# Optimization experiments

Hardware: AMD Instinct MI355X
Metric: run time of the kernel (lower is better)

## Reference

```python
import jax, jax.numpy as jnp
import numpy as np

INPUT, HIDDEN, C, H, W, PK = 64, 128, 16, 32, 32, 4
B, T = 512, 1024

def hardsigmoid(v):
    return jnp.clip(v / 6.0 + 0.5, 0.0, 1.0)

def setup_inputs() -> dict:
    key = jax.random.key(0)
    ks = jax.random.split(key, 9)
    s_rnn = 1.0 / np.sqrt(HIDDEN)
    s_map = 1.0 / np.sqrt(HIDDEN)
    return {
        "x": jax.random.normal(ks[0], (B, T, INPUT), dtype=jnp.float32),
        "W_ih": jax.random.uniform(ks[1], (HIDDEN, INPUT), minval=-s_rnn, maxval=s_rnn),
        "b_ih": jax.random.uniform(ks[2], (HIDDEN,), minval=-s_rnn, maxval=s_rnn),
        "W_hh": jax.random.uniform(ks[3], (HIDDEN, HIDDEN), minval=-s_rnn, maxval=s_rnn),
        "b_hh": jax.random.uniform(ks[4], (HIDDEN,), minval=-s_rnn, maxval=s_rnn),
        "W_gate": jax.random.uniform(ks[5], (HIDDEN, HIDDEN), minval=-s_rnn, maxval=s_rnn),
        "b_gate": jax.random.uniform(ks[6], (HIDDEN,), minval=-s_rnn, maxval=s_rnn),
        "W_map": jax.random.uniform(ks[7], (C * H * W, HIDDEN), minval=-s_map, maxval=s_map),
        "b_map": jax.random.uniform(ks[8], (C * H * W,), minval=-s_map, maxval=s_map),
    }

def reference(x, W_ih, b_ih, W_hh, b_hh, W_gate, b_gate, W_map, b_map):
    batch, seq_len, _ = x.shape
    h0 = jnp.zeros((batch, HIDDEN), dtype=x.dtype)
    agg0 = jnp.zeros((batch, HIDDEN), dtype=x.dtype)

    def step(carry, xt):
        h, agg = carry
        h = jnp.tanh(xt @ W_ih.T + b_ih + h @ W_hh.T + b_hh)
        gate = hardsigmoid(h @ W_gate.T + b_gate)
        return (h, agg + h * gate), None

    (h, agg), _ = jax.lax.scan(step, (h0, agg0), jnp.swapaxes(x, 0, 1))
    agg = agg / float(seq_len)

    mapped = (agg @ W_map.T + b_map).reshape(batch, C, H, W)
    # AvgPool2d(kernel=PK, stride=PK) via reshape-mean
    pooled = mapped.reshape(batch, C, H // PK, PK, W // PK, PK).mean(axis=(3, 5))
    upsampled = jnp.repeat(jnp.repeat(pooled, PK, axis=2), PK, axis=3)
    return mapped * hardsigmoid(upsampled)
```

## Files before the change

### kernel.cpp

```cpp
#include <hip/hip_runtime.h>
#include <hip/hip_bf16.h>

#define T_SEQ 1024
#define BATCH 512
#define INPUT 64
#define HID   128

typedef __attribute__((ext_vector_type(8))) short bf16x8;
typedef __attribute__((ext_vector_type(4))) short s16x4;
typedef __attribute__((ext_vector_type(4))) float f32x4;

__device__ __forceinline__ short f2bf(float f) {
    union { float f; unsigned u; } v; v.f = f;
    unsigned r = (v.u + 0x7FFFu + ((v.u >> 16) & 1u)) >> 16;
    return (short)r;
}

__device__ __forceinline__ float fast_tanh(float s) {
    float e = __expf(2.0f * s);
    return 1.0f - 2.0f * __builtin_amdgcn_rcpf(e + 1.0f);
}

__device__ __forceinline__ float hsig(float v) {
    return __builtin_amdgcn_fmed3f(v * 0.16666666666666666f + 0.5f, 0.0f, 1.0f);
}

__device__ __forceinline__ void wg_barrier_lds() {
    asm volatile("s_waitcnt lgkmcnt(0)" ::: "memory");
    __builtin_amdgcn_s_barrier();
    asm volatile("" ::: "memory");
}

__global__ __launch_bounds__(256) void cvt_kernel(const float* __restrict__ in,
                                                  short* __restrict__ out, int n4) {
    int i = blockIdx.x * 256 + threadIdx.x;
    if (i >= n4) return;
    f32x4 v = ((const f32x4*)in)[i];
    s16x4 o;
    #pragma unroll
    for (int j = 0; j < 4; ++j) o[j] = f2bf(v[j]);
    ((s16x4*)out)[i] = o;
}

template<bool PRE>
__global__ __launch_bounds__(512, 2) void rnn_kernel(
    const float* __restrict__ xf, const short* __restrict__ xb,
    const float* __restrict__ W_ih, const float* __restrict__ b_ih,
    const float* __restrict__ W_hh, const float* __restrict__ b_hh,
    const float* __restrict__ W_gate, const float* __restrict__ b_gate,
    float* __restrict__ agg_out)
{
    __shared__ short sh0[16][136];
    __shared__ short sh1[16][136];

    const int tid  = threadIdx.x;
    const int wave = tid >> 6, lane = tid & 63;
    const int q = lane >> 4, l15 = lane & 15;
    const int b0 = blockIdx.x * 16;
    const int n0 = wave * 16;
    const int n  = n0 + l15;

    bf16x8 w1[6], wg[4];
    #pragma unroll
    for (int kb = 0; kb < 6; ++kb) {
        const float* p = (kb < 2) ? (W_ih + n * INPUT + kb * 32 + q * 8)
                                  : (W_hh + n * HID + (kb - 2) * 32 + q * 8);
        bf16x8 f;
        #pragma unroll
        for (int j = 0; j < 8; ++j) f[j] = f2bf(p[j]);
        w1[kb] = f;
    }
    #pragma unroll
    for (int kb = 0; kb < 4; ++kb) {
        const float* p = W_gate + n * HID + kb * 32 + q * 8;
        bf16x8 f;
        #pragma unroll
        for (int j = 0; j < 8; ++j) f[j] = f2bf(p[j]);
        wg[kb] = f;
    }
    const float b1 = b_ih[n] + b_hh[n], bgv = b_gate[n];
    f32x4 bias1v, biasgv, zero4;
    #pragma unroll
    for (int r = 0; r < 4; ++r) { bias1v[r] = b1; biasgv[r] = bgv; zero4[r] = 0.0f; }

    f32x4 agg = zero4;
    float hp0 = 0.f, hp1 = 0.f, hp2 = 0.f, hp3 = 0.f;
    bf16x8 hf0, hf1, hf2, hf3;
    #pragma unroll
    for (int j = 0; j < 8; ++j) { hf0[j] = 0; hf1[j] = 0; hf2[j] = 0; hf3[j] = 0; }

    bf16x8 xaE0, xaE1, xaO0, xaO1;
    const short* xq = nullptr;
    const float* xqf = nullptr;
    if (PRE) {
        const short* xp = xb + ((long)(b0 + l15) * T_SEQ) * INPUT + q * 8;
        xaE0 = *(const bf16x8*)(xp);
        xaE1 = *(const bf16x8*)(xp + 32);
        xaO0 = *(const bf16x8*)(xp + INPUT);
        xaO1 = *(const bf16x8*)(xp + INPUT + 32);
        xq = xp + 2 * INPUT;
    } else {
        const float* xp = xf + ((long)(b0 + l15) * T_SEQ) * INPUT + q * 8;
        f32x4 a0 = *(const f32x4*)(xp),          a1 = *(const f32x4*)(xp + 4);
        f32x4 a2 = *(const f32x4*)(xp + 32),     a3 = *(const f32x4*)(xp + 36);
        f32x4 c0 = *(const f32x4*)(xp + 64),     c1 = *(const f32x4*)(xp + 68);
        f32x4 c2 = *(const f32x4*)(xp + 96),     c3 = *(const f32x4*)(xp + 100);
        #pragma unroll
        for (int j = 0; j < 4; ++j) {
            xaE0[j] = f2bf(a0[j]); xaE0[4 + j] = f2bf(a1[j]);
            xaE1[j] = f2bf(a2[j]); xaE1[4 + j] = f2bf(a3[j]);
            xaO0[j] = f2bf(c0[j]); xaO0[4 + j] = f2bf(c1[j]);
            xaO1[j] = f2bf(c2[j]); xaO1[4 + j] = f2bf(c3[j]);
        }
        xqf = xp + 2 * INPUT;
    }

    f32x4 accx;
    accx = __builtin_amdgcn_mfma_f32_16x16x32_bf16(xaE0, w1[0], bias1v, 0, 0, 0);
    accx = __builtin_amdgcn_mfma_f32_16x16x32_bf16(xaE1, w1[1], accx, 0, 0, 0);

    for (int i = 0; i < T_SEQ / 2; ++i) {
        {
            const int t = 2 * i;
            if (PRE) {
                xaE0 = *(const bf16x8*)(xq);
                xaE1 = *(const bf16x8*)(xq + 32);
                if (t < T_SEQ - 3) xq += INPUT;
            } else {
                f32x4 a0 = *(const f32x4*)(xqf),      a1 = *(const f32x4*)(xqf + 4);
                f32x4 a2 = *(const f32x4*)(xqf + 32), a3 = *(const f32x4*)(xqf + 36);
                #pragma unroll
                for (int j = 0; j < 4; ++j) {
                    xaE0[j] = f2bf(a0[j]); xaE0[4 + j] = f2bf(a1[j]);
                    xaE1[j] = f2bf(a2[j]); xaE1[4 + j] = f2bf(a3[j]);
                }
                if (t < T_SEQ - 3) xqf += INPUT;
            }

            f32x4 accA = __builtin_amdgcn_mfma_f32_16x16x32_bf16(hf0, w1[2], accx, 0, 0, 0);
            f32x4 accB = __builtin_amdgcn_mfma_f32_16x16x32_bf16(hf2, w1[4], zero4, 0, 0, 0);
            f32x4 gA   = __builtin_amdgcn_mfma_f32_16x16x32_bf16(hf0, wg[0], biasgv, 0, 0, 0);
            f32x4 gB   = __builtin_amdgcn_mfma_f32_16x16x32_bf16(hf2, wg[2], zero4, 0, 0, 0);
            accA = __builtin_amdgcn_mfma_f32_16x16x32_bf16(hf1, w1[3], accA, 0, 0, 0);
            accB = __builtin_amdgcn_mfma_f32_16x16x32_bf16(hf3, w1[5], accB, 0, 0, 0);
            gA   = __builtin_amdgcn_mfma_f32_16x16x32_bf16(hf1, wg[1], gA, 0, 0, 0);
            gB   = __builtin_amdgcn_mfma_f32_16x16x32_bf16(hf3, wg[3], gB, 0, 0, 0);
            accx = __builtin_amdgcn_mfma_f32_16x16x32_bf16(xaO0, w1[0], bias1v, 0, 0, 0);
            accx = __builtin_amdgcn_mfma_f32_16x16x32_bf16(xaO1, w1[1], accx, 0, 0, 0);

            float h0 = fast_tanh(accA[0] + accB[0]);
            float h1 = fast_tanh(accA[1] + accB[1]);
            float h2 = fast_tanh(accA[2] + accB[2]);
            float h3 = fast_tanh(accA[3] + accB[3]);
            agg[0] += hp0 * hsig(gA[0] + gB[0]);
            agg[1] += hp1 * hsig(gA[1] + gB[1]);
            agg[2] += hp2 * hsig(gA[2] + gB[2]);
            agg[3] += hp3 * hsig(gA[3] + gB[3]);

            sh0[q * 4 + 0][n] = f2bf(h0);
            sh0[q * 4 + 1][n] = f2bf(h1);
            sh0[q * 4 + 2][n] = f2bf(h2);
            sh0[q * 4 + 3][n] = f2bf(h3);
            wg_barrier_lds();
            hf0 = *(const bf16x8*)&sh0[l15][q * 8];
            hf1 = *(const bf16x8*)&sh0[l15][32 + q * 8];
            hf2 = *(const bf16x8*)&sh0[l15][64 + q * 8];
            hf3 = *(const bf16x8*)&sh0[l15][96 + q * 8];
            hp0 = h0; hp1 = h1; hp2 = h2; hp3 = h3;
        }
        {
            const int t = 2 * i + 1;
            if (PRE) {
                xaO0 = *(const bf16x8*)(xq);
                xaO1 = *(const bf16x8*)(xq + 32);
                if (t < T_SEQ - 3) xq += INPUT;
            } else {
                f32x4 a0 = *(const f32x4*)(xqf),      a1 = *(const f32x4*)(xqf + 4);
                f32x4 a2 = *(const f32x4*)(xqf + 32), a3 = *(const f32x4*)(xqf + 36);
                #pragma unroll
                for (int j = 0; j < 4; ++j) {
                    xaO0[j] = f2bf(a0[j]); xaO0[4 + j] = f2bf(a1[j]);
                    xaO1[j] = f2bf(a2[j]); xaO1[4 + j] = f2bf(a3[j]);
                }
                if (t < T_SEQ - 3) xqf += INPUT;
            }

            f32x4 accA = __builtin_amdgcn_mfma_f32_16x16x32_bf16(hf0, w1[2], accx, 0, 0, 0);
            f32x4 accB = __builtin_amdgcn_mfma_f32_16x16x32_bf16(hf2, w1[4], zero4, 0, 0, 0);
            f32x4 gA   = __builtin_amdgcn_mfma_f32_16x16x32_bf16(hf0, wg[0], biasgv, 0, 0, 0);
            f32x4 gB   = __builtin_amdgcn_mfma_f32_16x16x32_bf16(hf2, wg[2], zero4, 0, 0, 0);
            accA = __builtin_amdgcn_mfma_f32_16x16x32_bf16(hf1, w1[3], accA, 0, 0, 0);
            accB = __builtin_amdgcn_mfma_f32_16x16x32_bf16(hf3, w1[5], accB, 0, 0, 0);
            gA   = __builtin_amdgcn_mfma_f32_16x16x32_bf16(hf1, wg[1], gA, 0, 0, 0);
            gB   = __builtin_amdgcn_mfma_f32_16x16x32_bf16(hf3, wg[3], gB, 0, 0, 0);
            accx = __builtin_amdgcn_mfma_f32_16x16x32_bf16(xaE0, w1[0], bias1v, 0, 0, 0);
            accx = __builtin_amdgcn_mfma_f32_16x16x32_bf16(xaE1, w1[1], accx, 0, 0, 0);

            float h0 = fast_tanh(accA[0] + accB[0]);
            float h1 = fast_tanh(accA[1] + accB[1]);
            float h2 = fast_tanh(accA[2] + accB[2]);
            float h3 = fast_tanh(accA[3] + accB[3]);
            agg[0] += hp0 * hsig(gA[0] + gB[0]);
            agg[1] += hp1 * hsig(gA[1] + gB[1]);
            agg[2] += hp2 * hsig(gA[2] + gB[2]);
            agg[3] += hp3 * hsig(gA[3] + gB[3]);

            sh1[q * 4 + 0][n] = f2bf(h0);
            sh1[q * 4 + 1][n] = f2bf(h1);
            sh1[q * 4 + 2][n] = f2bf(h2);
            sh1[q * 4 + 3][n] = f2bf(h3);
            wg_barrier_lds();
            hf0 = *(const bf16x8*)&sh1[l15][q * 8];
            hf1 = *(const bf16x8*)&sh1[l15][32 + q * 8];
            hf2 = *(const bf16x8*)&sh1[l15][64 + q * 8];
            hf3 = *(const bf16x8*)&sh1[l15][96 + q * 8];
            hp0 = h0; hp1 = h1; hp2 = h2; hp3 = h3;
        }
    }

    f32x4 gA = __builtin_amdgcn_mfma_f32_16x16x32_bf16(hf0, wg[0], biasgv, 0, 0, 0);
    f32x4 gB = __builtin_amdgcn_mfma_f32_16x16x32_bf16(hf2, wg[2], zero4, 0, 0, 0);
    gA = __builtin_amdgcn_mfma_f32_16x16x32_bf16(hf1, wg[1], gA, 0, 0, 0);
    gB = __builtin_amdgcn_mfma_f32_16x16x32_bf16(hf3, wg[3], gB, 0, 0, 0);

    const float s = 1.0f / (float)T_SEQ;
    agg_out[(b0 + q * 4 + 0) * HID + n] = (agg[0] + hp0 * hsig(gA[0] + gB[0])) * s;
    agg_out[(b0 + q * 4 + 1) * HID + n] = (agg[1] + hp1 * hsig(gA[1] + gB[1])) * s;
    agg_out[(b0 + q * 4 + 2) * HID + n] = (agg[2] + hp2 * hsig(gA[2] + gB[2])) * s;
    agg_out[(b0 + q * 4 + 3) * HID + n] = (agg[3] + hp3 * hsig(gA[3] + gB[3])) * s;
}

template<bool PRE>
__global__ __launch_bounds__(256) void map_kernel(
    const float* __restrict__ agg, const float* __restrict__ Wf,
    const short* __restrict__ Wb, const float* __restrict__ b_map,
    float* __restrict__ mapped)
{
    const int tid  = threadIdx.x;
    const int wave = tid >> 6, lane = tid & 63;
    const int q = lane >> 4, l15 = lane & 15;
    const int mb = blockIdx.x & 31;
    const int nb = blockIdx.x >> 5;
    const int b0 = mb * 16;
    const int n0 = nb * 128 + wave * 32;

    bf16x8 af[4];
    #pragma unroll
    for (int kb = 0; kb < 4; ++kb) {
        const float* p = agg + (b0 + l15) * HID + kb * 32 + q * 8;
        bf16x8 f;
        #pragma unroll
        for (int j = 0; j < 8; ++j) f[j] = f2bf(p[j]);
        af[kb] = f;
    }
    #pragma unroll
    for (int tn = 0; tn < 2; ++tn) {
        int nn = n0 + tn * 16 + l15;
        float bias = b_map[nn];
        f32x4 c;
        #pragma unroll
        for (int r = 0; r < 4; ++r) c[r] = bias;
        #pragma unroll
        for (int kb = 0; kb < 4; ++kb) {
            bf16x8 f;
            if (PRE) {
                f = *(const bf16x8*)(Wb + (long)nn * HID + kb * 32 + q * 8);
            } else {
                const float* p = Wf + (long)nn * HID + kb * 32 + q * 8;
                #pragma unroll
                for (int j = 0; j < 8; ++j) f[j] = f2bf(p[j]);
            }
            c = __builtin_amdgcn_mfma_f32_16x16x32_bf16(af[kb], f, c, 0, 0, 0);
        }
        #pragma unroll
        for (int r = 0; r < 4; ++r)
            mapped[(long)(b0 + q * 4 + r) * 16384 + nn] = c[r];
    }
}

__global__ __launch_bounds__(256) void pool_gate_kernel(float* __restrict__ mapped)
{
    __shared__ float sh_part[256];
    __shared__ float sh_gate[64];
    const int tid = threadIdx.x;
    float* plane = mapped + (long)blockIdx.x * 1024;

    f32x4 m4 = *(const f32x4*)(plane + tid * 4);
    sh_part[tid] = m4[0] + m4[1] + m4[2] + m4[3];
    __syncthreads();
    if (tid < 64) {
        int ph = tid >> 3, pw = tid & 7;
        float s = 0.0f;
        #pragma unroll
        for (int i = 0; i < 4; ++i) s += sh_part[(4 * ph + i) * 8 + pw];
        sh_gate[tid] = hsig(s * (1.0f / 16.0f));
    }
    __syncthreads();
    int h = tid >> 3, wb = tid & 7;
    float g = sh_gate[(h >> 2) * 8 + wb];
    f32x4 o = m4 * g;
    *(f32x4*)(plane + tid * 4) = o;
}

extern "C" void kernel_launch(void* const* d_in, const int* in_sizes, int n_in,
                              void* d_out, int out_size, void* d_ws, size_t ws_size,
                              hipStream_t stream) {
    const float* x      = (const float*)d_in[0];
    const float* W_ih   = (const float*)d_in[1];
    const float* b_ih   = (const float*)d_in[2];
    const float* W_hh   = (const float*)d_in[3];
    const float* b_hh   = (const float*)d_in[4];
    const float* W_gate = (const float*)d_in[5];
    const float* b_gate = (const float*)d_in[6];
    const float* W_map  = (const float*)d_in[7];
    const float* b_map  = (const float*)d_in[8];
    float* out = (float*)d_out;

    const size_t xb_bytes = (size_t)BATCH * T_SEQ * INPUT * 2;
    const size_t wm_bytes = (size_t)16384 * HID * 2;
    const size_t agg_bytes = (size_t)BATCH * HID * 4;
    const bool pre = ws_size >= xb_bytes + wm_bytes + agg_bytes;

    if (pre) {
        short* x_bf  = (short*)d_ws;
        short* wm_bf = (short*)((char*)d_ws + xb_bytes);
        float* agg   = (float*)((char*)d_ws + xb_bytes + wm_bytes);

        cvt_kernel<<<(BATCH * T_SEQ * INPUT / 4 + 255) / 256, 256, 0, stream>>>(x, x_bf, BATCH * T_SEQ * INPUT / 4);
        cvt_kernel<<<(16384 * HID / 4 + 255) / 256, 256, 0, stream>>>(W_map, wm_bf, 16384 * HID / 4);
        rnn_kernel<true><<<32, 512, 0, stream>>>(x, x_bf, W_ih, b_ih, W_hh, b_hh,
                                                 W_gate, b_gate, agg);
        map_kernel<true><<<4096, 256, 0, stream>>>(agg, W_map, wm_bf, b_map, out);
    } else {
        float* agg = (float*)d_ws;
        rnn_kernel<false><<<32, 512, 0, stream>>>(x, nullptr, W_ih, b_ih, W_hh, b_hh,
                                                  W_gate, b_gate, agg);
        map_kernel<false><<<4096, 256, 0, stream>>>(agg, W_map, nullptr, b_map, out);
    }
    pool_gate_kernel<<<BATCH * 16, 256, 0, stream>>>(out);
}
```

Before: 717.5 us.

## Split RNN workgroup into two wave groups alternating recurrent and gate work

Restructures the recurrent kernel so the 8 waves form two groups of 4. Each wave now computes two 16-row output tiles with a transposed MFMA operand order. On alternating timesteps one group computes the critical h recurrence while the other computes the gate, the aggregate update and the next input projection, so that work leaves the serial critical path. h packing uses v_cvt_pk_bf16_f32 with vectorised LDS stores, and the two groups' partial aggregates are reduced through LDS at the end. The cost is two barriers per pair of steps and half the waves idle on the critical MFMA chain at any time.

```diff
diff --git a/kernel.cpp b/kernel.cpp
--- a/kernel.cpp
+++ b/kernel.cpp
@@ -9,11 +9,20 @@
 typedef __attribute__((ext_vector_type(8))) short bf16x8;
 typedef __attribute__((ext_vector_type(4))) short s16x4;
 typedef __attribute__((ext_vector_type(4))) float f32x4;
+typedef __attribute__((ext_vector_type(2))) unsigned int u32x2;
+
+#define MFMA __builtin_amdgcn_mfma_f32_16x16x32_bf16
 
 __device__ __forceinline__ short f2bf(float f) {
     union { float f; unsigned u; } v; v.f = f;
     unsigned r = (v.u + 0x7FFFu + ((v.u >> 16) & 1u)) >> 16;
     return (short)r;
+}
+
+__device__ __forceinline__ unsigned cvtpk_bf16(float lo, float hi) {
+    unsigned r;
+    asm("v_cvt_pk_bf16_f32 %0, %1, %2" : "=v"(r) : "v"(lo), "v"(hi));
+    return r;
 }
 
 __device__ __forceinline__ float fast_tanh(float s) {
@@ -44,190 +53,216 @@
 
 template<bool PRE>
 __global__ __launch_bounds__(512, 2) void rnn_kernel(
-    const float* __restrict__ xf, const short* __restrict__ xb,
+    const float* __restrict__ xf_, const short* __restrict__ xb,
     const float* __restrict__ W_ih, const float* __restrict__ b_ih,
     const float* __restrict__ W_hh, const float* __restrict__ b_hh,
     const float* __restrict__ W_gate, const float* __restrict__ b_gate,
     float* __restrict__ agg_out)
 {
-    __shared__ short sh0[16][136];
-    __shared__ short sh1[16][136];
+    __shared__ __align__(16) short sh[2][16][136];
 
     const int tid  = threadIdx.x;
     const int wave = tid >> 6, lane = tid & 63;
     const int q = lane >> 4, l15 = lane & 15;
     const int b0 = blockIdx.x * 16;
-    const int n0 = wave * 16;
-    const int n  = n0 + l15;
-
-    bf16x8 w1[6], wg[4];
-    #pragma unroll
-    for (int kb = 0; kb < 6; ++kb) {
-        const float* p = (kb < 2) ? (W_ih + n * INPUT + kb * 32 + q * 8)
-                                  : (W_hh + n * HID + (kb - 2) * 32 + q * 8);
-        bf16x8 f;
-        #pragma unroll
-        for (int j = 0; j < 8; ++j) f[j] = f2bf(p[j]);
-        w1[kb] = f;
-    }
-    #pragma unroll
-    for (int kb = 0; kb < 4; ++kb) {
-        const float* p = W_gate + n * HID + kb * 32 + q * 8;
-        bf16x8 f;
-        #pragma unroll
-        for (int j = 0; j < 8; ++j) f[j] = f2bf(p[j]);
-        wg[kb] = f;
-    }
-    const float b1 = b_ih[n] + b_hh[n], bgv = b_gate[n];
-    f32x4 bias1v, biasgv, zero4;
-    #pragma unroll
-    for (int r = 0; r < 4; ++r) { bias1v[r] = b1; biasgv[r] = bgv; zero4[r] = 0.0f; }
-
-    f32x4 agg = zero4;
-    float hp0 = 0.f, hp1 = 0.f, hp2 = 0.f, hp3 = 0.f;
-    bf16x8 hf0, hf1, hf2, hf3;
-    #pragma unroll
-    for (int j = 0; j < 8; ++j) { hf0[j] = 0; hf1[j] = 0; hf2[j] = 0; hf3[j] = 0; }
-
-    bf16x8 xaE0, xaE1, xaO0, xaO1;
-    const short* xq = nullptr;
-    const float* xqf = nullptr;
-    if (PRE) {
-        const short* xp = xb + ((long)(b0 + l15) * T_SEQ) * INPUT + q * 8;
-        xaE0 = *(const bf16x8*)(xp);
-        xaE1 = *(const bf16x8*)(xp + 32);
-        xaO0 = *(const bf16x8*)(xp + INPUT);
-        xaO1 = *(const bf16x8*)(xp + INPUT + 32);
-        xq = xp + 2 * INPUT;
+    const int group = wave >> 2;
+    const int gw = wave & 3;
+    const int R0 = 32 * gw, R1 = R0 + 16;
+
+    bf16x8 wih[2][2], whh[2][4], wgf[2][4];
+    #pragma unroll
+    for (int tile = 0; tile < 2; ++tile) {
+        const int row = (tile ? R1 : R0) + l15;
+        #pragma unroll
+        for (int f = 0; f < 2; ++f) {
+            const float* p = W_ih + row * INPUT + f * 32 + q * 8;
+            bf16x8 v;
+            #pragma unroll
+            for (int j = 0; j < 8; ++j) v[j] = f2bf(p[j]);
+            wih[tile][f] = v;
+        }
+        #pragma unroll
+        for (int f = 0; f < 4; ++f) {
+            const float* p = W_hh + row * HID + f * 32 + q * 8;
+            bf16x8 v;
+            #pragma unroll
+            for (int j = 0; j < 8; ++j) v[j] = f2bf(p[j]);
+            whh[tile][f] = v;
+        }
+        #pragma unroll
+        for (int f = 0; f < 4; ++f) {
+            const float* p = W_gate + row * HID + f * 32 + q * 8;
+            bf16x8 v;
+            #pragma unroll
+            for (int j = 0; j < 8; ++j) v[j] = f2bf(p[j]);
+            wgf[tile][f] = v;
+        }
+    }
+
+    f32x4 bias1[2], biasg[2], zero4;
+    #pragma unroll
+    for (int tile = 0; tile < 2; ++tile) {
+        const int rbase = (tile ? R1 : R0) + q * 4;
+        #pragma unroll
+        for (int r = 0; r < 4; ++r) {
+            bias1[tile][r] = b_ih[rbase + r] + b_hh[rbase + r];
+            biasg[tile][r] = b_gate[rbase + r];
+        }
+    }
+    #pragma unroll
+    for (int r = 0; r < 4; ++r) zero4[r] = 0.0f;
+
+    f32x4 agg0 = zero4, agg1 = zero4;
+    f32x4 hpA = zero4, hpB = zero4;
+    f32x4 accx0, accx1;
+    bf16x8 xf0, xf1;
+
+    const long lanebase = ((long)(b0 + l15) * T_SEQ) * INPUT + q * 8;
+    const short* xb_lane = PRE ? (xb + lanebase) : nullptr;
+    const float* xf_lane = PRE ? nullptr : (xf_ + lanebase);
+
+    auto load_x = [&](int tt) {
+        if constexpr (PRE) {
+            const short* p = xb_lane + (long)tt * INPUT;
+            xf0 = *(const bf16x8*)p;
+            xf1 = *(const bf16x8*)(p + 32);
+        } else {
+            const float* p = xf_lane + (long)tt * INPUT;
+            f32x4 a0 = *(const f32x4*)p,        a1 = *(const f32x4*)(p + 4);
+            f32x4 a2 = *(const f32x4*)(p + 32), a3 = *(const f32x4*)(p + 36);
+            #pragma unroll
+            for (int j = 0; j < 4; ++j) {
+                xf0[j] = f2bf(a0[j]); xf0[4 + j] = f2bf(a1[j]);
+                xf1[j] = f2bf(a2[j]); xf1[4 + j] = f2bf(a3[j]);
+            }
+        }
+    };
+
+    auto critical = [&](int t) {
+        const int rb = (t & 1) ^ 1, wb = t & 1;
+        bf16x8 hf0 = *(const bf16x8*)&sh[rb][l15][q * 8];
+        bf16x8 hf1 = *(const bf16x8*)&sh[rb][l15][32 + q * 8];
+        bf16x8 hf2 = *(const bf16x8*)&sh[rb][l15][64 + q * 8];
+        bf16x8 hf3 = *(const bf16x8*)&sh[rb][l15][96 + q * 8];
+        f32x4 a0 = MFMA(whh[0][0], hf0, accx0, 0, 0, 0);
+        f32x4 c0 = MFMA(whh[0][2], hf2, zero4, 0, 0, 0);
+        f32x4 a1 = MFMA(whh[1][0], hf0, accx1, 0, 0, 0);
+        f32x4 c1 = MFMA(whh[1][2], hf2, zero4, 0, 0, 0);
+        a0 = MFMA(whh[0][1], hf1, a0, 0, 0, 0);
+        c0 = MFMA(whh[0][3], hf3, c0, 0, 0, 0);
+        a1 = MFMA(whh[1][1], hf1, a1, 0, 0, 0);
+        c1 = MFMA(whh[1][3], hf3, c1, 0, 0, 0);
+        int tt = t + 2; if (tt > T_SEQ - 1) tt = T_SEQ - 1;
+        load_x(tt);
+        hpA[0] = fast_tanh(a0[0] + c0[0]);
+        hpA[1] = fast_tanh(a0[1] + c0[1]);
+        hpA[2] = fast_tanh(a0[2] + c0[2]);
+        hpA[3] = fast_tanh(a0[3] + c0[3]);
+        hpB[0] = fast_tanh(a1[0] + c1[0]);
+        hpB[1] = fast_tanh(a1[1] + c1[1]);
+        hpB[2] = fast_tanh(a1[2] + c1[2]);
+        hpB[3] = fast_tanh(a1[3] + c1[3]);
+        u32x2 p0, p1;
+        p0[0] = cvtpk_bf16(hpA[0], hpA[1]); p0[1] = cvtpk_bf16(hpA[2], hpA[3]);
+        p1[0] = cvtpk_bf16(hpB[0], hpB[1]); p1[1] = cvtpk_bf16(hpB[2], hpB[3]);
+        *(u32x2*)&sh[wb][l15][R0 + q * 4] = p0;
+        *(u32x2*)&sh[wb][l15][R1 + q * 4] = p1;
+    };
+
+    auto shadow = [&](int t) {
+        const int rb = (t & 1) ^ 1;
+        bf16x8 gf0 = *(const bf16x8*)&sh[rb][l15][q * 8];
+        bf16x8 gf1 = *(const bf16x8*)&sh[rb][l15][32 + q * 8];
+        bf16x8 gf2 = *(const bf16x8*)&sh[rb][l15][64 + q * 8];
+        bf16x8 gf3 = *(const bf16x8*)&sh[rb][l15][96 + q * 8];
+        f32x4 g0 = MFMA(wgf[0][0], gf0, biasg[0], 0, 0, 0);
+        f32x4 e0 = MFMA(wgf[0][2], gf2, zero4, 0, 0, 0);
+        f32x4 g1 = MFMA(wgf[1][0], gf0, biasg[1], 0, 0, 0);
+        f32x4 e1 = MFMA(wgf[1][2], gf2, zero4, 0, 0, 0);
+        g0 = MFMA(wgf[0][1], gf1, g0, 0, 0, 0);
+        e0 = MFMA(wgf[0][3], gf3, e0, 0, 0, 0);
+        g1 = MFMA(wgf[1][1], gf1, g1, 0, 0, 0);
+        e1 = MFMA(wgf[1][3], gf3, e1, 0, 0, 0);
+        accx0 = MFMA(wih[0][0], xf0, bias1[0], 0, 0, 0);
+        accx1 = MFMA(wih[1][0], xf0, bias1[1], 0, 0, 0);
+        accx0 = MFMA(wih[0][1], xf1, accx0, 0, 0, 0);
+        accx1 = MFMA(wih[1][1], xf1, accx1, 0, 0, 0);
+        #pragma unroll
+        for (int r = 0; r < 4; ++r) {
+            agg0[r] += hpA[r] * hsig(g0[r] + e0[r]);
+            agg1[r] += hpB[r] * hsig(g1[r] + e1[r]);
+        }
+    };
+
+    load_x(group);
+    accx0 = MFMA(wih[0][0], xf0, bias1[0], 0, 0, 0);
+    accx1 = MFMA(wih[1][0], xf0, bias1[1], 0, 0, 0);
+    accx0 = MFMA(wih[0][1], xf1, accx0, 0, 0, 0);
+    accx1 = MFMA(wih[1][1], xf1, accx1, 0, 0, 0);
+    if (group == 0) {
+        hpA[0] = fast_tanh(accx0[0]); hpA[1] = fast_tanh(accx0[1]);
+        hpA[2] = fast_tanh(accx0[2]); hpA[3] = fast_tanh(accx0[3]);
+        hpB[0] = fast_tanh(accx1[0]); hpB[1] = fast_tanh(accx1[1]);
+        hpB[2] = fast_tanh(accx1[2]); hpB[3] = fast_tanh(accx1[3]);
+        u32x2 p0, p1;
+        p0[0] = cvtpk_bf16(hpA[0], hpA[1]); p0[1] = cvtpk_bf16(hpA[2], hpA[3]);
+        p1[0] = cvtpk_bf16(hpB[0], hpB[1]); p1[1] = cvtpk_bf16(hpB[2], hpB[3]);
+        *(u32x2*)&sh[0][l15][R0 + q * 4] = p0;
+        *(u32x2*)&sh[0][l15][R1 + q * 4] = p1;
+        load_x(2);
+    }
+    wg_barrier_lds();
+
+    if (group == 0) {
+        for (int i = 0; i < 511; ++i) {
+            shadow(2 * i + 1);   wg_barrier_lds();
+            critical(2 * i + 2); wg_barrier_lds();
+        }
+        shadow(1023); wg_barrier_lds();
     } else {
-        const float* xp = xf + ((long)(b0 + l15) * T_SEQ) * INPUT + q * 8;
-        f32x4 a0 = *(const f32x4*)(xp),          a1 = *(const f32x4*)(xp + 4);
-        f32x4 a2 = *(const f32x4*)(xp + 32),     a3 = *(const f32x4*)(xp + 36);
-        f32x4 c0 = *(const f32x4*)(xp + 64),     c1 = *(const f32x4*)(xp + 68);
-        f32x4 c2 = *(const f32x4*)(xp + 96),     c3 = *(const f32x4*)(xp + 100);
-        #pragma unroll
-        for (int j = 0; j < 4; ++j) {
-            xaE0[j] = f2bf(a0[j]); xaE0[4 + j] = f2bf(a1[j]);
-            xaE1[j] = f2bf(a2[j]); xaE1[4 + j] = f2bf(a3[j]);
-            xaO0[j] = f2bf(c0[j]); xaO0[4 + j] = f2bf(c1[j]);
-            xaO1[j] = f2bf(c2[j]); xaO1[4 + j] = f2bf(c3[j]);
-        }
-        xqf = xp + 2 * INPUT;
-    }
-
-    f32x4 accx;
-    accx = __builtin_amdgcn_mfma_f32_16x16x32_bf16(xaE0, w1[0], bias1v, 0, 0, 0);
-    accx = __builtin_amdgcn_mfma_f32_16x16x32_bf16(xaE1, w1[1], accx, 0, 0, 0);
-
-    for (int i = 0; i < T_SEQ / 2; ++i) {
-        {
-            const int t = 2 * i;
-            if (PRE) {
-                xaE0 = *(const bf16x8*)(xq);
-                xaE1 = *(const bf16x8*)(xq + 32);
-                if (t < T_SEQ - 3) xq += INPUT;
-            } else {
-                f32x4 a0 = *(const f32x4*)(xqf),      a1 = *(const f32x4*)(xqf + 4);
-                f32x4 a2 = *(const f32x4*)(xqf + 32), a3 = *(const f32x4*)(xqf + 36);
-                #pragma unroll
-                for (int j = 0; j < 4; ++j) {
-                    xaE0[j] = f2bf(a0[j]); xaE0[4 + j] = f2bf(a1[j]);
-                    xaE1[j] = f2bf(a2[j]); xaE1[4 + j] = f2bf(a3[j]);
-                }
-                if (t < T_SEQ - 3) xqf += INPUT;
-            }
-
-            f32x4 accA = __builtin_amdgcn_mfma_f32_16x16x32_bf16(hf0, w1[2], accx, 0, 0, 0);
-            f32x4 accB = __builtin_amdgcn_mfma_f32_16x16x32_bf16(hf2, w1[4], zero4, 0, 0, 0);
-            f32x4 gA   = __builtin_amdgcn_mfma_f32_16x16x32_bf16(hf0, wg[0], biasgv, 0, 0, 0);
-            f32x4 gB   = __builtin_amdgcn_mfma_f32_16x16x32_bf16(hf2, wg[2], zero4, 0, 0, 0);
-            accA = __builtin_amdgcn_mfma_f32_16x16x32_bf16(hf1, w1[3], accA, 0, 0, 0);
-            accB = __builtin_amdgcn_mfma_f32_16x16x32_bf16(hf3, w1[5], accB, 0, 0, 0);
-            gA   = __builtin_amdgcn_mfma_f32_16x16x32_bf16(hf1, wg[1], gA, 0, 0, 0);
-            gB   = __builtin_amdgcn_mfma_f32_16x16x32_bf16(hf3, wg[3], gB, 0, 0, 0);
-            accx = __builtin_amdgcn_mfma_f32_16x16x32_bf16(xaO0, w1[0], bias1v, 0, 0, 0);
-            accx = __builtin_amdgcn_mfma_f32_16x16x32_bf16(xaO1, w1[1], accx, 0, 0, 0);
-
-            float h0 = fast_tanh(accA[0] + accB[0]);
-            float h1 = fast_tanh(accA[1] + accB[1]);
-            float h2 = fast_tanh(accA[2] + accB[2]);
-            float h3 = fast_tanh(accA[3] + accB[3]);
-            agg[0] += hp0 * hsig(gA[0] + gB[0]);
-            agg[1] += hp1 * hsig(gA[1] + gB[1]);
-            agg[2] += hp2 * hsig(gA[2] + gB[2]);
-            agg[3] += hp3 * hsig(gA[3] + gB[3]);
-
-            sh0[q * 4 + 0][n] = f2bf(h0);
-            sh0[q * 4 + 1][n] = f2bf(h1);
-            sh0[q * 4 + 2][n] = f2bf(h2);
-            sh0[q * 4 + 3][n] = f2bf(h3);
-            wg_barrier_lds();
-            hf0 = *(const bf16x8*)&sh0[l15][q * 8];
-            hf1 = *(const bf16x8*)&sh0[l15][32 + q * 8];
-            hf2 = *(const bf16x8*)&sh0[l15][64 + q * 8];
-            hf3 = *(const bf16x8*)&sh0[l15][96 + q * 8];
-            hp0 = h0; hp1 = h1; hp2 = h2; hp3 = h3;
-        }
-        {
-            const int t = 2 * i + 1;
-            if (PRE) {
-                xaO0 = *(const bf16x8*)(xq);
-                xaO1 = *(const bf16x8*)(xq + 32);
-                if (t < T_SEQ - 3) xq += INPUT;
-            } else {
-                f32x4 a0 = *(const f32x4*)(xqf),      a1 = *(const f32x4*)(xqf + 4);
-                f32x4 a2 = *(const f32x4*)(xqf + 32), a3 = *(const f32x4*)(xqf + 36);
-                #pragma unroll
-                for (int j = 0; j < 4; ++j) {
-                    xaO0[j] = f2bf(a0[j]); xaO0[4 + j] = f2bf(a1[j]);
-                    xaO1[j] = f2bf(a2[j]); xaO1[4 + j] = f2bf(a3[j]);
-                }
-                if (t < T_SEQ - 3) xqf += INPUT;
-            }
-
-            f32x4 accA = __builtin_amdgcn_mfma_f32_16x16x32_bf16(hf0, w1[2], accx, 0, 0, 0);
-            f32x4 accB = __builtin_amdgcn_mfma_f32_16x16x32_bf16(hf2, w1[4], zero4, 0, 0, 0);
-            f32x4 gA   = __builtin_amdgcn_mfma_f32_16x16x32_bf16(hf0, wg[0], biasgv, 0, 0, 0);
-            f32x4 gB   = __builtin_amdgcn_mfma_f32_16x16x32_bf16(hf2, wg[2], zero4, 0, 0, 0);
-            accA = __builtin_amdgcn_mfma_f32_16x16x32_bf16(hf1, w1[3], accA, 0, 0, 0);
-            accB = __builtin_amdgcn_mfma_f32_16x16x32_bf16(hf3, w1[5], accB, 0, 0, 0);
-            gA   = __builtin_amdgcn_mfma_f32_16x16x32_bf16(hf1, wg[1], gA, 0, 0, 0);
-            gB   = __builtin_amdgcn_mfma_f32_16x16x32_bf16(hf3, wg[3], gB, 0, 0, 0);
-            accx = __builtin_amdgcn_mfma_f32_16x16x32_bf16(xaE0, w1[0], bias1v, 0, 0, 0);
-            accx = __builtin_amdgcn_mfma_f32_16x16x32_bf16(xaE1, w1[1], accx, 0, 0, 0);
-
-            float h0 = fast_tanh(accA[0] + accB[0]);
-            float h1 = fast_tanh(accA[1] + accB[1]);
-            float h2 = fast_tanh(accA[2] + accB[2]);
-            float h3 = fast_tanh(accA[3] + accB[3]);
-            agg[0] += hp0 * hsig(gA[0] + gB[0]);
-            agg[1] += hp1 * hsig(gA[1] + gB[1]);
-            agg[2] += hp2 * hsig(gA[2] + gB[2]);
-            agg[3] += hp3 * hsig(gA[3] + gB[3]);
-
-            sh1[q * 4 + 0][n] = f2bf(h0);
-            sh1[q * 4 + 1][n] = f2bf(h1);
-            sh1[q * 4 + 2][n] = f2bf(h2);
-            sh1[q * 4 + 3][n] = f2bf(h3);
-            wg_barrier_lds();
-            hf0 = *(const bf16x8*)&sh1[l15][q * 8];
-            hf1 = *(const bf16x8*)&sh1[l15][32 + q * 8];
-            hf2 = *(const bf16x8*)&sh1[l15][64 + q * 8];
-            hf3 = *(const bf16x8*)&sh1[l15][96 + q * 8];
-            hp0 = h0; hp1 = h1; hp2 = h2; hp3 = h3;
-        }
-    }
-
-    f32x4 gA = __builtin_amdgcn_mfma_f32_16x16x32_bf16(hf0, wg[0], biasgv, 0, 0, 0);
-    f32x4 gB = __builtin_amdgcn_mfma_f32_16x16x32_bf16(hf2, wg[2], zero4, 0, 0, 0);
-    gA = __builtin_amdgcn_mfma_f32_16x16x32_bf16(hf1, wg[1], gA, 0, 0, 0);
-    gB = __builtin_amdgcn_mfma_f32_16x16x32_bf16(hf3, wg[3], gB, 0, 0, 0);
-
-    const float s = 1.0f / (float)T_SEQ;
-    agg_out[(b0 + q * 4 + 0) * HID + n] = (agg[0] + hp0 * hsig(gA[0] + gB[0])) * s;
-    agg_out[(b0 + q * 4 + 1) * HID + n] = (agg[1] + hp1 * hsig(gA[1] + gB[1])) * s;
-    agg_out[(b0 + q * 4 + 2) * HID + n] = (agg[2] + hp2 * hsig(gA[2] + gB[2])) * s;
-    agg_out[(b0 + q * 4 + 3) * HID + n] = (agg[3] + hp3 * hsig(gA[3] + gB[3])) * s;
+        for (int i = 0; i < 511; ++i) {
+            critical(2 * i + 1); wg_barrier_lds();
+            shadow(2 * i + 2);   wg_barrier_lds();
+        }
+        critical(1023); wg_barrier_lds();
+    }
+
+    if (group == 1) {
+        bf16x8 gf0 = *(const bf16x8*)&sh[1][l15][q * 8];
+        bf16x8 gf1 = *(const bf16x8*)&sh[1][l15][32 + q * 8];
+        bf16x8 gf2 = *(const bf16x8*)&sh[1][l15][64 + q * 8];
+        bf16x8 gf3 = *(const bf16x8*)&sh[1][l15][96 + q * 8];
+        f32x4 g0 = MFMA(wgf[0][0], gf0, biasg[0], 0, 0, 0);
+        f32x4 e0 = MFMA(wgf[0][2], gf2, zero4, 0, 0, 0);
+        f32x4 g1 = MFMA(wgf[1][0], gf0, biasg[1], 0, 0, 0);
+        f32x4 e1 = MFMA(wgf[1][2], gf2, zero4, 0, 0, 0);
+        g0 = MFMA(wgf[0][1], gf1, g0, 0, 0, 0);
+        e0 = MFMA(wgf[0][3], gf3, e0, 0, 0, 0);
+        g1 = MFMA(wgf[1][1], gf1, g1, 0, 0, 0);
+        e1 = MFMA(wgf[1][3], gf3, e1, 0, 0, 0);
+        #pragma unroll
+        for (int r = 0; r < 4; ++r) {
+            agg0[r] += hpA[r] * hsig(g0[r] + e0[r]);
+            agg1[r] += hpB[r] * hsig(g1[r] + e1[r]);
+        }
+    }
+    wg_barrier_lds();
+
+    float* aggf = (float*)&sh[0][0][0];
+    if (group == 0) {
+        *(f32x4*)&aggf[l15 * HID + R0 + q * 4] = agg0;
+        *(f32x4*)&aggf[l15 * HID + R1 + q * 4] = agg1;
+    }
+    wg_barrier_lds();
+    if (group == 1) {
+        const float s = 1.0f / (float)T_SEQ;
+        f32x4 t0 = *(const f32x4*)&aggf[l15 * HID + R0 + q * 4];
+        f32x4 t1 = *(const f32x4*)&aggf[l15 * HID + R1 + q * 4];
+        #pragma unroll
+        for (int r = 0; r < 4; ++r) { t0[r] = (t0[r] + agg0[r]) * s; t1[r] = (t1[r] + agg1[r]) * s; }
+        *(f32x4*)&agg_out[(long)(b0 + l15) * HID + R0 + q * 4] = t0;
+        *(f32x4*)&agg_out[(long)(b0 + l15) * HID + R1 + q * 4] = t1;
+    }
 }
 
 template<bool PRE>
```

After: 694.7 us. 3.2% less time.
